# Optimization experiments

Measured on AMD Instinct MI355X. Metric: run time of the kernel, lower is better.

Reference implementation:

```python
import jax, jax.numpy as jnp
import numpy as np

N_NODES = 50000
N_EDGES = 1600000
D_IN = 128
D_HID = 128
D_OUT = 128


def setup_inputs() -> dict:
    key = jax.random.key(0)
    k1, k2, k3, k4, k5, k6 = jax.random.split(key, 6)
    x = jax.random.normal(k1, (N_NODES, D_IN), dtype=jnp.float32)
    edge_index = jax.random.randint(k2, (2, N_EDGES), 0, N_NODES, dtype=jnp.int64)
    # glorot-ish init for GCNConv linear weights; bias zeros-like but randomized small
    W1 = jax.random.normal(k3, (D_IN, D_HID), dtype=jnp.float32) * (1.0 / np.sqrt(D_IN))
    b1 = jax.random.normal(k4, (D_HID,), dtype=jnp.float32) * 0.01
    W2 = jax.random.normal(k5, (D_HID, D_OUT), dtype=jnp.float32) * (1.0 / np.sqrt(D_HID))
    b2 = jax.random.normal(k6, (D_OUT,), dtype=jnp.float32) * 0.01
    return {"x": x, "edge_index": edge_index, "W1": W1, "b1": b1, "W2": W2, "b2": b2}


def gcn_conv(x, src, dst, W, b, n_nodes):
    # PyG GCNConv: add self-loops, symmetric normalization deg^-1/2, lin -> aggregate -> +bias
    loop = jnp.arange(n_nodes, dtype=src.dtype)
    s = jnp.concatenate([src, loop])  # [E+N]
    d = jnp.concatenate([dst, loop])  # [E+N]
    deg = jax.ops.segment_sum(jnp.ones_like(d, dtype=x.dtype), d, num_segments=n_nodes)
    dinv = jnp.where(deg > 0, jax.lax.rsqrt(deg), 0.0)
    norm = dinv[s] * dinv[d]  # [E+N]
    h = x @ W  # [N, F_out]
    msg = h[s] * norm[:, None]  # gather + scale: [E+N, F_out]
    out = jax.ops.segment_sum(msg, d, num_segments=n_nodes)  # scatter-add
    return out + b


def reference(x, edge_index, W1, b1, W2, b2):
    src, dst = edge_index[0], edge_index[1]
    h = gcn_conv(x, src, dst, W1, b1, N_NODES)
    h = jnp.where(h >= 0, h, 0.1 * h)  # LeakyReLU(0.1)
    h = gcn_conv(h, src, dst, W2, b2, N_NODES)
    return h.mean(axis=1)  # [N]
```

## Files before the change

### kernel.cpp

```cpp
#include <hip/hip_runtime.h>
#include <hip/hip_bf16.h>


#define N_NODES 50000
#define NPAD 50048
#define D 128
#define BK 196
#define CHUNK 4096

typedef unsigned int uint;
typedef unsigned short u16;
typedef __attribute__((ext_vector_type(8))) short short8;
typedef __attribute__((ext_vector_type(4))) float floatx4;

__device__ __forceinline__ u16 cvt_bf16(float f) {
    uint u = __float_as_uint(f);
    return (u16)((u + 0x7fffu + ((u >> 16) & 1u)) >> 16);
}
__device__ __forceinline__ uint pack_bf2(float a, float b) {
    return (uint)cvt_bf16(a) | ((uint)cvt_bf16(b) << 16);
}

__global__ void hist_kernel(const int* __restrict__ dst, uint* __restrict__ H, int E, int CHN) {
    __shared__ uint h[BK];
    int t = threadIdx.x, c = blockIdx.x;
    if (t < BK) h[t] = 0;
    __syncthreads();
    int e0 = c * CHUNK;
    for (int i = t; i < CHUNK; i += 256) {
        int e = e0 + i;
        if (e < E) atomicAdd(&h[dst[e] >> 8], 1u);
    }
    __syncthreads();
    if (t < BK) H[t * CHN + c] = h[t];
}

__global__ void colscan_kernel(uint* __restrict__ H, uint* __restrict__ T, int CHN) {
    __shared__ uint s[256];
    int t = threadIdx.x, b = blockIdx.x;
    uint carry = 0;
    for (int base = 0; base < CHN; base += 256) {
        int idx = base + t;
        uint v = (idx < CHN) ? H[b * CHN + idx] : 0u;
        s[t] = v;
        __syncthreads();
#pragma unroll
        for (int off = 1; off < 256; off <<= 1) {
            uint u = (t >= off) ? s[t - off] : 0u;
            __syncthreads();
            s[t] += u;
            __syncthreads();
        }
        if (idx < CHN) H[b * CHN + idx] = carry + s[t] - v;
        carry += s[255];
        __syncthreads();
    }
    if (t == 0) T[b] = carry;
}

__global__ void totscan_kernel(const uint* __restrict__ T, uint* __restrict__ B,
                               int* __restrict__ row, int E, int N) {
    __shared__ uint s[256];
    int t = threadIdx.x;
    uint v = (t < BK) ? T[t] : 0u;
    s[t] = v;
    __syncthreads();
#pragma unroll
    for (int off = 1; off < 256; off <<= 1) {
        uint u = (t >= off) ? s[t - off] : 0u;
        __syncthreads();
        s[t] += u;
        __syncthreads();
    }
    if (t < BK) B[t] = s[t] - v;
    if (t == 0) { B[BK] = (uint)E; row[N] = E; }
}

__global__ void scatter_kernel(const int* __restrict__ src, const int* __restrict__ dst,
                               const uint* __restrict__ H, const uint* __restrict__ B,
                               uint* __restrict__ EB, int E, int CHN) {
    __shared__ uint cur[BK];
    int t = threadIdx.x, c = blockIdx.x;
    if (t < BK) cur[t] = B[t] + H[t * CHN + c];
    __syncthreads();
    int e0 = c * CHUNK;
    for (int i = t; i < CHUNK; i += 256) {
        int e = e0 + i;
        if (e < E) {
            int d = dst[e];
            uint slot = atomicAdd(&cur[d >> 8], 1u);
            EB[slot] = ((uint)(d & 255) << 16) | (uint)src[e];
        }
    }
}

__global__ void bucket_sort_kernel(const uint* __restrict__ EB, const uint* __restrict__ B,
                                   int* __restrict__ row, float* __restrict__ dinv,
                                   u16* __restrict__ esrc, int N) {
    __shared__ uint cnt[256], s[256], cur[256];
    int t = threadIdx.x, b = blockIdx.x;
    uint base = B[b], ne = B[b + 1] - base;
    cnt[t] = 0;
    __syncthreads();
    for (uint i = t; i < ne; i += 256) atomicAdd(&cnt[EB[base + i] >> 16], 1u);
    __syncthreads();
    uint c = cnt[t];
    s[t] = c;
    __syncthreads();
#pragma unroll
    for (int off = 1; off < 256; off <<= 1) {
        uint u = (t >= off) ? s[t - off] : 0u;
        __syncthreads();
        s[t] += u;
        __syncthreads();
    }
    uint p = s[t] - c;
    int v = (b << 8) + t;
    if (v < N) {
        row[v] = (int)(base + p);
        dinv[v] = rsqrtf((float)(c + 1u));
    }
    cur[t] = base + p;
    __syncthreads();
    for (uint i = t; i < ne; i += 256) {
        uint u = EB[base + i];
        uint slot = atomicAdd(&cur[u >> 16], 1u);
        esrc[slot] = (u16)(u & 0xffffu);
    }
}

__global__ void w2m_kernel(const float* __restrict__ W2, const float* __restrict__ b2,
                           float* __restrict__ w2m) {
    int k = blockIdx.x, lane = threadIdx.x;
    const float* p = (k < 128) ? (W2 + k * 128) : b2;
    float s = p[lane] + p[lane + 64];
#pragma unroll
    for (int off = 32; off > 0; off >>= 1) s += __shfl_down(s, off, 64);
    if (lane == 0) w2m[k] = s * (1.0f / 128.0f);
}

#define WT_STRIDE 136
__global__ __launch_bounds__(256) void gemm_mfma_kernel(
    const float* __restrict__ A, const float* __restrict__ W,
    u16* __restrict__ G16, const float* __restrict__ dinv, int M) {
    __shared__ u16 Wt[128 * WT_STRIDE];
    int t = threadIdx.x;
    for (int i = t; i < 128 * 128; i += 256) {
        int k = i >> 7, n = i & 127;
        Wt[n * WT_STRIDE + k] = cvt_bf16(W[i]);
    }
    __syncthreads();

    int wave = t >> 6, lane = t & 63;
    int m = lane & 15, quad = lane >> 4;
    int rowa = blockIdx.x * 64 + wave * 16 + m;
    int rowc = rowa < M ? rowa : M - 1;
    const float* Arow = A + (long)rowc * D;

    short8 afrag[4];
#pragma unroll
    for (int kt = 0; kt < 4; kt++) {
        int k0 = kt * 32 + quad * 8;
        float4 f0 = *(const float4*)(Arow + k0);
        float4 f1 = *(const float4*)(Arow + k0 + 4);
        short8 af;
        af[0] = (short)cvt_bf16(f0.x); af[1] = (short)cvt_bf16(f0.y);
        af[2] = (short)cvt_bf16(f0.z); af[3] = (short)cvt_bf16(f0.w);
        af[4] = (short)cvt_bf16(f1.x); af[5] = (short)cvt_bf16(f1.y);
        af[6] = (short)cvt_bf16(f1.z); af[7] = (short)cvt_bf16(f1.w);
        afrag[kt] = af;
    }

    int orow0 = blockIdx.x * 64 + wave * 16;
    float dv[4]; bool ok[4];
#pragma unroll
    for (int r = 0; r < 4; r++) {
        int orow = orow0 + quad * 4 + r;
        ok[r] = orow < M;
        dv[r] = dinv[ok[r] ? orow : (M - 1)];
    }

    uint* G32 = (uint*)G16;
    for (int n0 = 0; n0 < 128; n0 += 16) {
        floatx4 acc = {0.f, 0.f, 0.f, 0.f};
#pragma unroll
        for (int kt = 0; kt < 4; kt++) {
            short8 bf = *(const short8*)(Wt + (n0 + m) * WT_STRIDE + kt * 32 + quad * 8);
            acc = __builtin_amdgcn_mfma_f32_16x16x32_bf16(afrag[kt], bf, acc, 0, 0, 0);
        }
#pragma unroll
        for (int r = 0; r < 4; r++) {
            float val = acc[r] * dv[r];
            float oth = __shfl_xor(val, 1, 64);
            if (ok[r] && (m & 1) == 0) {
                int orow = orow0 + quad * 4 + r;
                G32[(long)orow * 64 + ((n0 + m) >> 1)] = pack_bf2(val, oth);
            }
        }
    }
}

__global__ __launch_bounds__(256) void gather_node_kernel(
    const int* __restrict__ row, const u16* __restrict__ esrc,
    const uint* __restrict__ g16, const float* __restrict__ dinv,
    const float* __restrict__ b1, const float* __restrict__ w2m,
    float* __restrict__ mg, int N) {
    int wave = threadIdx.x >> 6;
    int lane = threadIdx.x & 63;
    int sub = lane & 7;
    int nb = lane >> 3;
    int v = blockIdx.x * 4 + wave;
    if (v >= N) return;

    const uint4* gv = (const uint4*)g16;
    float acc[16];
#pragma unroll
    for (int i = 0; i < 16; i++) acc[i] = 0.f;

#define ACC8(ua, ub) {                                                   \
    uint uu[8] = {(ua).x, (ua).y, (ua).z, (ua).w, (ub).x, (ub).y, (ub).z, (ub).w}; \
    _Pragma("unroll")                                                    \
    for (int i = 0; i < 8; i++) {                                        \
        acc[2*i]   += __uint_as_float(uu[i] << 16);                      \
        acc[2*i+1] += __uint_as_float(uu[i] & 0xffff0000u);              \
    } }

    if (nb == 0) {
        long rb = (long)v * 16 + 2 * sub;
        uint4 ua = gv[rb], ub = gv[rb + 1];
        ACC8(ua, ub)
    }
    int jb = row[v], je = row[v + 1];
    int j = jb + nb;
    if (j < je) {
        long r0 = (long)esrc[j] * 16 + 2 * sub;
        uint4 p0 = gv[r0], p1 = gv[r0 + 1];
        j += 8;
        while (j < je) {
            long r1 = (long)esrc[j] * 16 + 2 * sub;
            uint4 q0 = gv[r1], q1 = gv[r1 + 1];
            j += 8;
            ACC8(p0, p1)
            p0 = q0; p1 = q1;
        }
        ACC8(p0, p1)
    }
#undef ACC8

#pragma unroll
    for (int i = 0; i < 16; i++) {
        acc[i] += __shfl_xor(acc[i], 8, 64);
        acc[i] += __shfl_xor(acc[i], 16, 64);
        acc[i] += __shfl_xor(acc[i], 32, 64);
    }

    if (nb == 0) {
        float dvv = dinv[v];
        const float4* bp = (const float4*)b1;
        const float4* wp = (const float4*)w2m;
        float s = 0.f;
#pragma unroll
        for (int q4 = 0; q4 < 4; q4++) {
            float4 bb = bp[sub * 4 + q4];
            float4 wm = wp[sub * 4 + q4];
            float t0 = dvv * acc[4*q4 + 0] + bb.x; t0 = t0 >= 0.f ? t0 : 0.1f * t0;
            float t1 = dvv * acc[4*q4 + 1] + bb.y; t1 = t1 >= 0.f ? t1 : 0.1f * t1;
            float t2 = dvv * acc[4*q4 + 2] + bb.z; t2 = t2 >= 0.f ? t2 : 0.1f * t2;
            float t3 = dvv * acc[4*q4 + 3] + bb.w; t3 = t3 >= 0.f ? t3 : 0.1f * t3;
            s += t0 * wm.x + t1 * wm.y + t2 * wm.z + t3 * wm.w;
        }
        s += __shfl_xor(s, 1, 64);
        s += __shfl_xor(s, 2, 64);
        s += __shfl_xor(s, 4, 64);
        if (sub == 0) mg[v] = dvv * s;
    }
}

__global__ void out_kernel(const int* __restrict__ row, const u16* __restrict__ esrc,
                           const float* __restrict__ mg, const float* __restrict__ dinv,
                           const float* __restrict__ w2m, float* __restrict__ out, int N) {
    int v = blockIdx.x * blockDim.x + threadIdx.x;
    if (v >= N) return;
    float acc = mg[v];
    int jb = row[v], je = row[v + 1];
    int j = jb;
    for (; j + 8 <= je; j += 8) {
        acc += mg[esrc[j]] + mg[esrc[j + 1]] + mg[esrc[j + 2]] + mg[esrc[j + 3]] +
               mg[esrc[j + 4]] + mg[esrc[j + 5]] + mg[esrc[j + 6]] + mg[esrc[j + 7]];
    }
    for (; j < je; j++) acc += mg[esrc[j]];
    out[v] = dinv[v] * acc + w2m[128];
}

extern "C" void kernel_launch(void* const* d_in, const int* in_sizes, int n_in,
                              void* d_out, int out_size, void* d_ws, size_t ws_size,
                              hipStream_t stream) {
    const float* x  = (const float*)d_in[0];
    const int* ei   = (const int*)d_in[1];
    const float* W1 = (const float*)d_in[2];
    const float* b1 = (const float*)d_in[3];
    const float* W2 = (const float*)d_in[4];
    const float* b2 = (const float*)d_in[5];
    float* out = (float*)d_out;

    const int N = N_NODES;
    const int E = in_sizes[1] / 2;
    const int* src = ei;
    const int* dst = ei + E;
    const int CHN = (E + CHUNK - 1) / CHUNK;
    const int nblocks = (N + 255) / 256;

    float*    dinv = (float*)d_ws;
    int*      row  = (int*)(dinv + NPAD);
    uint*     B    = (uint*)(row + NPAD + 16);
    float*    w2m  = (float*)(B + 256);
    float*    mg   = w2m + 256;
    uint*     T    = (uint*)(mg + NPAD);
    uint*     g16u = T + 256;
    u16*      esrc = (u16*)(g16u + NPAD * 64);
    uint*     H    = (uint*)(esrc + E + (E & 1));
    uint*     EB   = g16u;

    hist_kernel<<<CHN, 256, 0, stream>>>(dst, H, E, CHN);
    colscan_kernel<<<BK, 256, 0, stream>>>(H, T, CHN);
    totscan_kernel<<<1, 256, 0, stream>>>(T, B, row, E, N);
    scatter_kernel<<<CHN, 256, 0, stream>>>(src, dst, H, B, EB, E, CHN);
    bucket_sort_kernel<<<BK, 256, 0, stream>>>(EB, B, row, dinv, esrc, N);

    w2m_kernel<<<129, 64, 0, stream>>>(W2, b2, w2m);

    gemm_mfma_kernel<<<(N + 63) / 64, 256, 0, stream>>>(x, W1, (u16*)g16u, dinv, N);

    gather_node_kernel<<<(N + 3) / 4, 256, 0, stream>>>(row, esrc, g16u, dinv, b1, w2m, mg, N);

    out_kernel<<<nblocks, 256, 0, stream>>>(row, esrc, mg, dinv, w2m, out, N);
}
```

Baseline: 217.1 us.

## Split feature matrix into column quarters and gather each quarter separately

The GEMM output is stored as four column slices of 32 features, each a contiguous [NPAD x 16 uint] array. The gather kernel launches one block per node-quarter pair, so each gathered row is a 64-byte segment from a smaller array that is more likely to stay cached, and each wave runs 16 edge chains instead of 8. Each block writes a partial dot product per quarter, and a new small kernel combines the four partials into mg. The cost is four times as many gather blocks re-reading the edge lists, an extra kernel launch, and a partial buffer.

```diff
diff --git a/kernel.cpp b/kernel.cpp
--- a/kernel.cpp
+++ b/kernel.cpp
@@ -142,7 +142,7 @@
 #define WT_STRIDE 136
 __global__ __launch_bounds__(256) void gemm_mfma_kernel(
     const float* __restrict__ A, const float* __restrict__ W,
-    u16* __restrict__ G16, const float* __restrict__ dinv, int M) {
+    uint* __restrict__ G32, const float* __restrict__ dinv, int M) {
     __shared__ u16 Wt[128 * WT_STRIDE];
     int t = threadIdx.x;
     for (int i = t; i < 128 * 128; i += 256) {
@@ -180,7 +180,6 @@
         dv[r] = dinv[ok[r] ? orow : (M - 1)];
     }
 
-    uint* G32 = (uint*)G16;
     for (int n0 = 0; n0 < 128; n0 += 16) {
         floatx4 acc = {0.f, 0.f, 0.f, 0.f};
 #pragma unroll
@@ -194,86 +193,91 @@
             float oth = __shfl_xor(val, 1, 64);
             if (ok[r] && (m & 1) == 0) {
                 int orow = orow0 + quad * 4 + r;
-                G32[(long)orow * 64 + ((n0 + m) >> 1)] = pack_bf2(val, oth);
+                int c = n0 + m;
+                G32[(long)(c >> 5) * NPAD * 16 + (long)orow * 16 + ((c & 31) >> 1)]
+                    = pack_bf2(val, oth);
             }
         }
     }
 }
 
-__global__ __launch_bounds__(256) void gather_node_kernel(
+__global__ __launch_bounds__(256) void gather_q_kernel(
     const int* __restrict__ row, const u16* __restrict__ esrc,
     const uint* __restrict__ g16, const float* __restrict__ dinv,
     const float* __restrict__ b1, const float* __restrict__ w2m,
-    float* __restrict__ mg, int N) {
+    float* __restrict__ partial, int N) {
+    int b = blockIdx.x;
+    int slot = b & 7;
+    int q = slot >> 1;
     int wave = threadIdx.x >> 6;
     int lane = threadIdx.x & 63;
-    int sub = lane & 7;
-    int nb = lane >> 3;
-    int v = blockIdx.x * 4 + wave;
+    int v = (b >> 3) * 8 + (slot & 1) * 4 + wave;
     if (v >= N) return;
-
-    const uint4* gv = (const uint4*)g16;
-    float acc[16];
-#pragma unroll
-    for (int i = 0; i < 16; i++) acc[i] = 0.f;
-
-#define ACC8(ua, ub) {                                                   \
-    uint uu[8] = {(ua).x, (ua).y, (ua).z, (ua).w, (ub).x, (ub).y, (ub).z, (ub).w}; \
-    _Pragma("unroll")                                                    \
-    for (int i = 0; i < 8; i++) {                                        \
-        acc[2*i]   += __uint_as_float(uu[i] << 16);                      \
-        acc[2*i+1] += __uint_as_float(uu[i] & 0xffff0000u);              \
-    } }
-
-    if (nb == 0) {
-        long rb = (long)v * 16 + 2 * sub;
-        uint4 ua = gv[rb], ub = gv[rb + 1];
-        ACC8(ua, ub)
+    int chain = lane >> 2, p = lane & 3;
+
+    const uint4* gq = (const uint4*)(g16 + (long)q * NPAD * 16);
+    float acc[8];
+#pragma unroll
+    for (int i = 0; i < 8; i++) acc[i] = 0.f;
+
+#define ACC4(u) {                                                        \
+    acc[0] += __uint_as_float((u).x << 16); acc[1] += __uint_as_float((u).x & 0xffff0000u); \
+    acc[2] += __uint_as_float((u).y << 16); acc[3] += __uint_as_float((u).y & 0xffff0000u); \
+    acc[4] += __uint_as_float((u).z << 16); acc[5] += __uint_as_float((u).z & 0xffff0000u); \
+    acc[6] += __uint_as_float((u).w << 16); acc[7] += __uint_as_float((u).w & 0xffff0000u); }
+
+    if (chain == 0) {
+        uint4 u = gq[(long)v * 4 + p];
+        ACC4(u)
     }
     int jb = row[v], je = row[v + 1];
-    int j = jb + nb;
+    int j = jb + chain;
     if (j < je) {
-        long r0 = (long)esrc[j] * 16 + 2 * sub;
-        uint4 p0 = gv[r0], p1 = gv[r0 + 1];
-        j += 8;
+        int s0 = (int)__builtin_nontemporal_load(&esrc[j]);
+        uint4 u0 = gq[(long)s0 * 4 + p];
+        j += 16;
         while (j < je) {
-            long r1 = (long)esrc[j] * 16 + 2 * sub;
-            uint4 q0 = gv[r1], q1 = gv[r1 + 1];
-            j += 8;
-            ACC8(p0, p1)
-            p0 = q0; p1 = q1;
-        }
-        ACC8(p0, p1)
-    }
-#undef ACC8
-
-#pragma unroll
-    for (int i = 0; i < 16; i++) {
+            int s1 = (int)__builtin_nontemporal_load(&esrc[j]);
+            uint4 u1 = gq[(long)s1 * 4 + p];
+            j += 16;
+            ACC4(u0)
+            u0 = u1;
+        }
+        ACC4(u0)
+    }
+#undef ACC4
+
+#pragma unroll
+    for (int i = 0; i < 8; i++) {
+        acc[i] += __shfl_xor(acc[i], 4, 64);
         acc[i] += __shfl_xor(acc[i], 8, 64);
         acc[i] += __shfl_xor(acc[i], 16, 64);
         acc[i] += __shfl_xor(acc[i], 32, 64);
     }
 
-    if (nb == 0) {
-        float dvv = dinv[v];
-        const float4* bp = (const float4*)b1;
-        const float4* wp = (const float4*)w2m;
-        float s = 0.f;
-#pragma unroll
-        for (int q4 = 0; q4 < 4; q4++) {
-            float4 bb = bp[sub * 4 + q4];
-            float4 wm = wp[sub * 4 + q4];
-            float t0 = dvv * acc[4*q4 + 0] + bb.x; t0 = t0 >= 0.f ? t0 : 0.1f * t0;
-            float t1 = dvv * acc[4*q4 + 1] + bb.y; t1 = t1 >= 0.f ? t1 : 0.1f * t1;
-            float t2 = dvv * acc[4*q4 + 2] + bb.z; t2 = t2 >= 0.f ? t2 : 0.1f * t2;
-            float t3 = dvv * acc[4*q4 + 3] + bb.w; t3 = t3 >= 0.f ? t3 : 0.1f * t3;
-            s += t0 * wm.x + t1 * wm.y + t2 * wm.z + t3 * wm.w;
-        }
-        s += __shfl_xor(s, 1, 64);
-        s += __shfl_xor(s, 2, 64);
-        s += __shfl_xor(s, 4, 64);
-        if (sub == 0) mg[v] = dvv * s;
-    }
+    float dvv = dinv[v];
+    const float2* bp = (const float2*)b1;
+    const float2* wp = (const float2*)w2m;
+    float s = 0.f;
+#pragma unroll
+    for (int k = 0; k < 4; k++) {
+        float2 bb = bp[q * 16 + p * 4 + k];
+        float2 wm = wp[q * 16 + p * 4 + k];
+        float t0 = dvv * acc[2 * k]     + bb.x; t0 = t0 >= 0.f ? t0 : 0.1f * t0;
+        float t1 = dvv * acc[2 * k + 1] + bb.y; t1 = t1 >= 0.f ? t1 : 0.1f * t1;
+        s += t0 * wm.x + t1 * wm.y;
+    }
+    s += __shfl_xor(s, 1, 64);
+    s += __shfl_xor(s, 2, 64);
+    if (lane == 0) partial[q * NPAD + v] = s;
+}
+
+__global__ void mg_kernel(const float* __restrict__ partial, const float* __restrict__ dinv,
+                          float* __restrict__ mg, int N) {
+    int v = blockIdx.x * blockDim.x + threadIdx.x;
+    if (v >= N) return;
+    mg[v] = dinv[v] * (partial[v] + partial[NPAD + v] +
+                       partial[2 * NPAD + v] + partial[3 * NPAD + v]);
 }
 
 __global__ void out_kernel(const int* __restrict__ row, const u16* __restrict__ esrc,
@@ -310,16 +314,17 @@
     const int CHN = (E + CHUNK - 1) / CHUNK;
     const int nblocks = (N + 255) / 256;
 
-    float*    dinv = (float*)d_ws;
-    int*      row  = (int*)(dinv + NPAD);
-    uint*     B    = (uint*)(row + NPAD + 16);
-    float*    w2m  = (float*)(B + 256);
-    float*    mg   = w2m + 256;
-    uint*     T    = (uint*)(mg + NPAD);
-    uint*     g16u = T + 256;
-    u16*      esrc = (u16*)(g16u + NPAD * 64);
-    uint*     H    = (uint*)(esrc + E + (E & 1));
-    uint*     EB   = g16u;
+    float*    dinv    = (float*)d_ws;
+    int*      row     = (int*)(dinv + NPAD);
+    uint*     B       = (uint*)(row + NPAD + 16);
+    float*    w2m     = (float*)(B + 256);
+    float*    mg      = w2m + 256;
+    uint*     T       = (uint*)(mg + NPAD);
+    float*    partial = (float*)(T + 256);
+    uint*     g16u    = (uint*)(partial + 4 * NPAD);
+    u16*      esrc    = (u16*)(g16u + NPAD * 64);
+    uint*     H       = (uint*)(esrc + E + (E & 1));
+    uint*     EB      = g16u;
 
     hist_kernel<<<CHN, 256, 0, stream>>>(dst, H, E, CHN);
     colscan_kernel<<<BK, 256, 0, stream>>>(H, T, CHN);
@@ -329,9 +334,11 @@
 
     w2m_kernel<<<129, 64, 0, stream>>>(W2, b2, w2m);
 
-    gemm_mfma_kernel<<<(N + 63) / 64, 256, 0, stream>>>(x, W1, (u16*)g16u, dinv, N);
-
-    gather_node_kernel<<<(N + 3) / 4, 256, 0, stream>>>(row, esrc, g16u, dinv, b1, w2m, mg, N);
+    gemm_mfma_kernel<<<(N + 63) / 64, 256, 0, stream>>>(x, W1, g16u, dinv, N);
+
+    gather_q_kernel<<<N, 256, 0, stream>>>(row, esrc, g16u, dinv, b1, w2m, partial, N);
+
+    mg_kernel<<<nblocks, 256, 0, stream>>>(partial, dinv, mg, N);
 
     out_kernel<<<nblocks, 256, 0, stream>>>(row, esrc, mg, dinv, w2m, out, N);
 }
```

Result: slower. 251.9 us (+16.0%).

## Fuse preprocessing kernels and move source dinv scaling into gather

Applied to the files above, without the earlier changes.

Merges the histogram with the W2 row-mean computation, and merges the column scan and total scan into one kernel using a last-block ticket counter. Bucket sort and the MFMA GEMM now run as independent blocks of a single launch, which requires removing the GEMM's dependency on dinv. The gather kernel applies dinv[src] per edge instead, which adds a scattered dinv load per edge, and EB gets its own buffer instead of aliasing g16. The aim is to cut kernel launches and the serialization between stages.

```diff
diff --git a/kernel.cpp b/kernel.cpp
--- a/kernel.cpp
+++ b/kernel.cpp
@@ -21,22 +21,42 @@
     return (uint)cvt_bf16(a) | ((uint)cvt_bf16(b) << 16);
 }
 
-__global__ void hist_kernel(const int* __restrict__ dst, uint* __restrict__ H, int E, int CHN) {
-    __shared__ uint h[BK];
+__global__ void hist_w2m_kernel(const int* __restrict__ dst, uint* __restrict__ H,
+                                const float* __restrict__ W2, const float* __restrict__ b2,
+                                float* __restrict__ w2m, uint* __restrict__ counter,
+                                int E, int CHN) {
     int t = threadIdx.x, c = blockIdx.x;
-    if (t < BK) h[t] = 0;
-    __syncthreads();
-    int e0 = c * CHUNK;
-    for (int i = t; i < CHUNK; i += 256) {
-        int e = e0 + i;
-        if (e < E) atomicAdd(&h[dst[e] >> 8], 1u);
-    }
-    __syncthreads();
-    if (t < BK) H[t * CHN + c] = h[t];
-}
-
-__global__ void colscan_kernel(uint* __restrict__ H, uint* __restrict__ T, int CHN) {
+    if (c < CHN) {
+        __shared__ uint h[BK];
+        if (t < BK) h[t] = 0;
+        __syncthreads();
+        int e0 = c * CHUNK;
+        for (int i = t; i < CHUNK; i += 256) {
+            int e = e0 + i;
+            if (e < E) atomicAdd(&h[dst[e] >> 8], 1u);
+        }
+        __syncthreads();
+        if (t < BK) H[t * CHN + c] = h[t];
+    } else {
+        if (t < 128) {
+            float s = 0.f;
+            for (int j = 0; j < 128; j++) s += W2[t * 128 + j];
+            w2m[t] = s * (1.0f / 128.0f);
+        } else if (t == 128) {
+            float s = 0.f;
+            for (int j = 0; j < 128; j++) s += b2[j];
+            w2m[128] = s * (1.0f / 128.0f);
+        } else if (t == 129) {
+            *counter = 0;
+        }
+    }
+}
+
+__global__ void scan_kernel(uint* __restrict__ H, uint* __restrict__ T, uint* __restrict__ B,
+                            int* __restrict__ row, uint* __restrict__ counter,
+                            int CHN, int E, int N) {
     __shared__ uint s[256];
+    __shared__ uint ticket_sh;
     int t = threadIdx.x, b = blockIdx.x;
     uint carry = 0;
     for (int base = 0; base < CHN; base += 256) {
@@ -55,25 +75,27 @@
         carry += s[255];
         __syncthreads();
     }
-    if (t == 0) T[b] = carry;
-}
-
-__global__ void totscan_kernel(const uint* __restrict__ T, uint* __restrict__ B,
-                               int* __restrict__ row, int E, int N) {
-    __shared__ uint s[256];
-    int t = threadIdx.x;
-    uint v = (t < BK) ? T[t] : 0u;
-    s[t] = v;
+    if (t == 0) {
+        atomicExch(&T[b], carry);
+        __threadfence();
+        ticket_sh = atomicAdd(counter, 1);
+    }
     __syncthreads();
-#pragma unroll
-    for (int off = 1; off < 256; off <<= 1) {
-        uint u = (t >= off) ? s[t - off] : 0u;
-        __syncthreads();
-        s[t] += u;
-        __syncthreads();
-    }
-    if (t < BK) B[t] = s[t] - v;
-    if (t == 0) { B[BK] = (uint)E; row[N] = E; }
+    if (ticket_sh == (uint)(gridDim.x - 1)) {
+        __threadfence();
+        uint v = (t < BK) ? atomicAdd(&T[t], 0u) : 0u;
+        s[t] = v;
+        __syncthreads();
+#pragma unroll
+        for (int off = 1; off < 256; off <<= 1) {
+            uint u = (t >= off) ? s[t - off] : 0u;
+            __syncthreads();
+            s[t] += u;
+            __syncthreads();
+        }
+        if (t < BK) B[t] = s[t] - v;
+        if (t == 0) { B[BK] = (uint)E; row[N] = E; }
+    }
 }
 
 __global__ void scatter_kernel(const int* __restrict__ src, const int* __restrict__ dst,
@@ -94,107 +116,92 @@
     }
 }
 
-__global__ void bucket_sort_kernel(const uint* __restrict__ EB, const uint* __restrict__ B,
-                                   int* __restrict__ row, float* __restrict__ dinv,
-                                   u16* __restrict__ esrc, int N) {
-    __shared__ uint cnt[256], s[256], cur[256];
-    int t = threadIdx.x, b = blockIdx.x;
-    uint base = B[b], ne = B[b + 1] - base;
-    cnt[t] = 0;
-    __syncthreads();
-    for (uint i = t; i < ne; i += 256) atomicAdd(&cnt[EB[base + i] >> 16], 1u);
-    __syncthreads();
-    uint c = cnt[t];
-    s[t] = c;
-    __syncthreads();
-#pragma unroll
-    for (int off = 1; off < 256; off <<= 1) {
-        uint u = (t >= off) ? s[t - off] : 0u;
-        __syncthreads();
-        s[t] += u;
-        __syncthreads();
-    }
-    uint p = s[t] - c;
-    int v = (b << 8) + t;
-    if (v < N) {
-        row[v] = (int)(base + p);
-        dinv[v] = rsqrtf((float)(c + 1u));
-    }
-    cur[t] = base + p;
-    __syncthreads();
-    for (uint i = t; i < ne; i += 256) {
-        uint u = EB[base + i];
-        uint slot = atomicAdd(&cur[u >> 16], 1u);
-        esrc[slot] = (u16)(u & 0xffffu);
-    }
-}
-
-__global__ void w2m_kernel(const float* __restrict__ W2, const float* __restrict__ b2,
-                           float* __restrict__ w2m) {
-    int k = blockIdx.x, lane = threadIdx.x;
-    const float* p = (k < 128) ? (W2 + k * 128) : b2;
-    float s = p[lane] + p[lane + 64];
-#pragma unroll
-    for (int off = 32; off > 0; off >>= 1) s += __shfl_down(s, off, 64);
-    if (lane == 0) w2m[k] = s * (1.0f / 128.0f);
-}
-
 #define WT_STRIDE 136
-__global__ __launch_bounds__(256) void gemm_mfma_kernel(
+union SortGemmSmem {
+    struct { uint cnt[256], s[256], cur[256]; } sort;
+    u16 wt[128 * WT_STRIDE];
+};
+__global__ __launch_bounds__(256) void sortgemm_kernel(
+    const uint* __restrict__ EB, const uint* __restrict__ B,
+    int* __restrict__ row, float* __restrict__ dinv, u16* __restrict__ esrc,
     const float* __restrict__ A, const float* __restrict__ W,
-    u16* __restrict__ G16, const float* __restrict__ dinv, int M) {
-    __shared__ u16 Wt[128 * WT_STRIDE];
+    uint* __restrict__ G32, int N, int M) {
+    __shared__ SortGemmSmem sm;
     int t = threadIdx.x;
-    for (int i = t; i < 128 * 128; i += 256) {
-        int k = i >> 7, n = i & 127;
-        Wt[n * WT_STRIDE + k] = cvt_bf16(W[i]);
-    }
-    __syncthreads();
-
-    int wave = t >> 6, lane = t & 63;
-    int m = lane & 15, quad = lane >> 4;
-    int rowa = blockIdx.x * 64 + wave * 16 + m;
-    int rowc = rowa < M ? rowa : M - 1;
-    const float* Arow = A + (long)rowc * D;
-
-    short8 afrag[4];
-#pragma unroll
-    for (int kt = 0; kt < 4; kt++) {
-        int k0 = kt * 32 + quad * 8;
-        float4 f0 = *(const float4*)(Arow + k0);
-        float4 f1 = *(const float4*)(Arow + k0 + 4);
-        short8 af;
-        af[0] = (short)cvt_bf16(f0.x); af[1] = (short)cvt_bf16(f0.y);
-        af[2] = (short)cvt_bf16(f0.z); af[3] = (short)cvt_bf16(f0.w);
-        af[4] = (short)cvt_bf16(f1.x); af[5] = (short)cvt_bf16(f1.y);
-        af[6] = (short)cvt_bf16(f1.z); af[7] = (short)cvt_bf16(f1.w);
-        afrag[kt] = af;
-    }
-
-    int orow0 = blockIdx.x * 64 + wave * 16;
-    float dv[4]; bool ok[4];
-#pragma unroll
-    for (int r = 0; r < 4; r++) {
-        int orow = orow0 + quad * 4 + r;
-        ok[r] = orow < M;
-        dv[r] = dinv[ok[r] ? orow : (M - 1)];
-    }
-
-    uint* G32 = (uint*)G16;
-    for (int n0 = 0; n0 < 128; n0 += 16) {
-        floatx4 acc = {0.f, 0.f, 0.f, 0.f};
+
+    if (blockIdx.x < BK) {
+        int b = blockIdx.x;
+        uint base = B[b], ne = B[b + 1] - base;
+        sm.sort.cnt[t] = 0;
+        __syncthreads();
+        for (uint i = t; i < ne; i += 256) atomicAdd(&sm.sort.cnt[EB[base + i] >> 16], 1u);
+        __syncthreads();
+        uint c = sm.sort.cnt[t];
+        sm.sort.s[t] = c;
+        __syncthreads();
+#pragma unroll
+        for (int off = 1; off < 256; off <<= 1) {
+            uint u = (t >= off) ? sm.sort.s[t - off] : 0u;
+            __syncthreads();
+            sm.sort.s[t] += u;
+            __syncthreads();
+        }
+        uint p = sm.sort.s[t] - c;
+        int v = (b << 8) + t;
+        if (v < N) {
+            row[v] = (int)(base + p);
+            dinv[v] = rsqrtf((float)(c + 1u));
+        }
+        sm.sort.cur[t] = base + p;
+        __syncthreads();
+        for (uint i = t; i < ne; i += 256) {
+            uint u = EB[base + i];
+            uint slot = atomicAdd(&sm.sort.cur[u >> 16], 1u);
+            esrc[slot] = (u16)(u & 0xffffu);
+        }
+    } else {
+        int bid = blockIdx.x - BK;
+        for (int i = t; i < 128 * 128; i += 256) {
+            int k = i >> 7, n = i & 127;
+            sm.wt[n * WT_STRIDE + k] = cvt_bf16(W[i]);
+        }
+        __syncthreads();
+
+        int wave = t >> 6, lane = t & 63;
+        int m = lane & 15, quad = lane >> 4;
+        int rowa = bid * 64 + wave * 16 + m;
+        int rowc = rowa < M ? rowa : M - 1;
+        const float* Arow = A + (long)rowc * D;
+
+        short8 afrag[4];
 #pragma unroll
         for (int kt = 0; kt < 4; kt++) {
-            short8 bf = *(const short8*)(Wt + (n0 + m) * WT_STRIDE + kt * 32 + quad * 8);
-            acc = __builtin_amdgcn_mfma_f32_16x16x32_bf16(afrag[kt], bf, acc, 0, 0, 0);
-        }
-#pragma unroll
-        for (int r = 0; r < 4; r++) {
-            float val = acc[r] * dv[r];
-            float oth = __shfl_xor(val, 1, 64);
-            if (ok[r] && (m & 1) == 0) {
+            int k0 = kt * 32 + quad * 8;
+            float4 f0 = *(const float4*)(Arow + k0);
+            float4 f1 = *(const float4*)(Arow + k0 + 4);
+            short8 af;
+            af[0] = (short)cvt_bf16(f0.x); af[1] = (short)cvt_bf16(f0.y);
+            af[2] = (short)cvt_bf16(f0.z); af[3] = (short)cvt_bf16(f0.w);
+            af[4] = (short)cvt_bf16(f1.x); af[5] = (short)cvt_bf16(f1.y);
+            af[6] = (short)cvt_bf16(f1.z); af[7] = (short)cvt_bf16(f1.w);
+            afrag[kt] = af;
+        }
+
+        int orow0 = bid * 64 + wave * 16;
+        for (int n0 = 0; n0 < 128; n0 += 16) {
+            floatx4 acc = {0.f, 0.f, 0.f, 0.f};
+#pragma unroll
+            for (int kt = 0; kt < 4; kt++) {
+                short8 bf = *(const short8*)(sm.wt + (n0 + m) * WT_STRIDE + kt * 32 + quad * 8);
+                acc = __builtin_amdgcn_mfma_f32_16x16x32_bf16(afrag[kt], bf, acc, 0, 0, 0);
+            }
+#pragma unroll
+            for (int r = 0; r < 4; r++) {
+                float val = acc[r];
+                float oth = __shfl_xor(val, 1, 64);
                 int orow = orow0 + quad * 4 + r;
-                G32[(long)orow * 64 + ((n0 + m) >> 1)] = pack_bf2(val, oth);
+                if (orow < M && (m & 1) == 0)
+                    G32[(long)orow * 64 + ((n0 + m) >> 1)] = pack_bf2(val, oth);
             }
         }
     }
@@ -213,37 +220,42 @@
     if (v >= N) return;
 
     const uint4* gv = (const uint4*)g16;
+    float dvv = dinv[v];
     float acc[16];
 #pragma unroll
     for (int i = 0; i < 16; i++) acc[i] = 0.f;
 
-#define ACC8(ua, ub) {                                                   \
+#define ACC8(ua, ub, wgt) {                                              \
     uint uu[8] = {(ua).x, (ua).y, (ua).z, (ua).w, (ub).x, (ub).y, (ub).z, (ub).w}; \
     _Pragma("unroll")                                                    \
     for (int i = 0; i < 8; i++) {                                        \
-        acc[2*i]   += __uint_as_float(uu[i] << 16);                      \
-        acc[2*i+1] += __uint_as_float(uu[i] & 0xffff0000u);              \
+        acc[2*i]   += (wgt) * __uint_as_float(uu[i] << 16);              \
+        acc[2*i+1] += (wgt) * __uint_as_float(uu[i] & 0xffff0000u);      \
     } }
 
     if (nb == 0) {
         long rb = (long)v * 16 + 2 * sub;
         uint4 ua = gv[rb], ub = gv[rb + 1];
-        ACC8(ua, ub)
+        ACC8(ua, ub, dvv)
     }
     int jb = row[v], je = row[v + 1];
     int j = jb + nb;
     if (j < je) {
-        long r0 = (long)esrc[j] * 16 + 2 * sub;
+        int s0 = esrc[j];
+        float wA = dinv[s0];
+        long r0 = (long)s0 * 16 + 2 * sub;
         uint4 p0 = gv[r0], p1 = gv[r0 + 1];
         j += 8;
         while (j < je) {
-            long r1 = (long)esrc[j] * 16 + 2 * sub;
+            int s1 = esrc[j];
+            float wB = dinv[s1];
+            long r1 = (long)s1 * 16 + 2 * sub;
             uint4 q0 = gv[r1], q1 = gv[r1 + 1];
             j += 8;
-            ACC8(p0, p1)
-            p0 = q0; p1 = q1;
-        }
-        ACC8(p0, p1)
+            ACC8(p0, p1, wA)
+            p0 = q0; p1 = q1; wA = wB;
+        }
+        ACC8(p0, p1, wA)
     }
 #undef ACC8
 
@@ -255,7 +267,6 @@
     }
 
     if (nb == 0) {
-        float dvv = dinv[v];
         const float4* bp = (const float4*)b1;
         const float4* wp = (const float4*)w2m;
         float s = 0.f;
@@ -310,28 +321,23 @@
     const int CHN = (E + CHUNK - 1) / CHUNK;
     const int nblocks = (N + 255) / 256;
 
-    float*    dinv = (float*)d_ws;
-    int*      row  = (int*)(dinv + NPAD);
-    uint*     B    = (uint*)(row + NPAD + 16);
-    float*    w2m  = (float*)(B + 256);
-    float*    mg   = w2m + 256;
-    uint*     T    = (uint*)(mg + NPAD);
-    uint*     g16u = T + 256;
-    u16*      esrc = (u16*)(g16u + NPAD * 64);
-    uint*     H    = (uint*)(esrc + E + (E & 1));
-    uint*     EB   = g16u;
-
-    hist_kernel<<<CHN, 256, 0, stream>>>(dst, H, E, CHN);
-    colscan_kernel<<<BK, 256, 0, stream>>>(H, T, CHN);
-    totscan_kernel<<<1, 256, 0, stream>>>(T, B, row, E, N);
+    float*    dinv    = (float*)d_ws;
+    int*      row     = (int*)(dinv + NPAD);
+    uint*     B       = (uint*)(row + NPAD + 16);
+    float*    w2m     = (float*)(B + 256);
+    float*    mg      = w2m + 256;
+    uint*     T       = (uint*)(mg + NPAD);
+    uint*     counter = T + 256;
+    uint*     g16u    = counter + 16;
+    u16*      esrc    = (u16*)(g16u + (long)NPAD * 64);
+    uint*     H       = (uint*)(esrc + E);
+    uint*     EB      = H + BK * CHN;
+
+    hist_w2m_kernel<<<CHN + 1, 256, 0, stream>>>(dst, H, W2, b2, w2m, counter, E, CHN);
+    scan_kernel<<<BK, 256, 0, stream>>>(H, T, B, row, counter, CHN, E, N);
     scatter_kernel<<<CHN, 256, 0, stream>>>(src, dst, H, B, EB, E, CHN);
-    bucket_sort_kernel<<<BK, 256, 0, stream>>>(EB, B, row, dinv, esrc, N);
-
-    w2m_kernel<<<129, 64, 0, stream>>>(W2, b2, w2m);
-
-    gemm_mfma_kernel<<<(N + 63) / 64, 256, 0, stream>>>(x, W1, (u16*)g16u, dinv, N);
-
+    sortgemm_kernel<<<BK + (N + 63) / 64, 256, 0, stream>>>(EB, B, row, dinv, esrc,
+                                                            x, W1, g16u, N, N);
     gather_node_kernel<<<(N + 3) / 4, 256, 0, stream>>>(row, esrc, g16u, dinv, b1, w2m, mg, N);
-
     out_kernel<<<nblocks, 256, 0, stream>>>(row, esrc, mg, dinv, w2m, out, N);
 }
```

Result: faster. 196.1 us (-9.7%).
